# Kernel tuning notes

Measured on AMD Instinct MI355X. Metric: run time of the kernel, lower is better.

Reference implementation:

```python
import jax, jax.numpy as jnp
import numpy as np

N_NODES = 50000
N_EDGES = 1200000
IN_FEATS = 64
OUT_FEATS = 64
NEG_SLOPE = 0.01  # F.leaky_relu default


def setup_inputs() -> dict:
    key = jax.random.key(0)
    k1, k2, k3, k4, k5, k6 = jax.random.split(key, 6)
    feature = jax.random.normal(k1, (N_NODES, IN_FEATS), dtype=jnp.float32)
    attn_w = jax.random.normal(k2, (2 * IN_FEATS, 1), dtype=jnp.float32) * 0.1
    lin_w = jax.random.normal(k3, (OUT_FEATS, 2 * IN_FEATS), dtype=jnp.float32) * 0.1
    lin_b = jax.random.normal(k4, (OUT_FEATS,), dtype=jnp.float32) * 0.1
    src = jax.random.randint(k5, (N_EDGES,), 0, N_NODES, dtype=jnp.int32)
    dst = jax.random.randint(k6, (N_EDGES,), 0, N_NODES, dtype=jnp.int32)
    return {"feature": feature, "attn_w": attn_w, "lin_w": lin_w,
            "lin_b": lin_b, "src": src, "dst": dst}


def reference(feature, attn_w, lin_w, lin_b, src, dst):
    N = feature.shape[0]
    # edge attention: leaky_relu(attn_fc([h_src, h_dst]))
    # split attn weight to avoid materializing the [E, 2*in] concat
    a_src, a_dst = attn_w[:IN_FEATS, 0], attn_w[IN_FEATS:, 0]
    e = jax.nn.leaky_relu(feature[src] @ a_src + feature[dst] @ a_dst,
                          negative_slope=NEG_SLOPE)  # [E]
    # segment softmax over incoming edges of each destination node
    emax = jax.ops.segment_max(e, dst, num_segments=N)
    emax = jnp.where(jnp.isfinite(emax), emax, 0.0)  # guard empty segments
    ex = jnp.exp(e - emax[dst])                       # [E]
    denom = jax.ops.segment_sum(ex, dst, num_segments=N)          # [N]
    num = jax.ops.segment_sum(ex[:, None] * feature[src], dst,
                              num_segments=N)                      # [N, in]
    hm = jnp.where(denom[:, None] > 0, num / denom[:, None], 0.0)
    # node apply: relu(Linear([h, hm]))
    h = jnp.concatenate([feature, hm], axis=1) @ lin_w.T + lin_b
    return jax.nn.relu(h)
```

## Files before the change

kernel.cpp:

```cpp
#include <hip/hip_runtime.h>
#include <math.h>

#define N_NODES 50000
#define N_EDGES 1200000
#define F 64
#define CAP 49
#define BSTR2 56
#define OVF_MAX 1024
#define NBIN 782
#define BSTR 16
#define CAP_BIN 2304
#define TILE 8192
#define NTILE ((N_EDGES + TILE - 1) / TILE)
#define XSTR 72

typedef __attribute__((ext_vector_type(8))) short short8;
typedef __attribute__((ext_vector_type(4))) float v4f;


__device__ __forceinline__ unsigned short f32_to_bf16_rne(float f) {
    unsigned u = __float_as_uint(f);
    return (unsigned short)((u + 0x7FFFu + ((u >> 16) & 1u)) >> 16);
}

__global__ void k_prep(const float* __restrict__ feature,
                       const float* __restrict__ attn_w,
                       float* __restrict__ s, float* __restrict__ dd,
                       unsigned short* __restrict__ fb,
                       unsigned* __restrict__ fq32) {
    int gid = blockIdx.x * blockDim.x + threadIdx.x;
    int wave = gid >> 6;
    int lane = threadIdx.x & 63;
    if (wave >= N_NODES) return;
    float f = feature[wave * F + lane];
    fb[wave * F + lane] = f32_to_bf16_rne(f);
    if (lane < 16) {
        float4 x = ((const float4*)(feature + (size_t)wave * F))[lane];
        int pk0 = __builtin_amdgcn_cvt_pk_fp8_f32(x.x, x.y, 0, false);
        int pkw = __builtin_amdgcn_cvt_pk_fp8_f32(x.z, x.w, pk0, true);
        fq32[wave * 16 + lane] = (unsigned)pkw;
    }
    float sv = f * attn_w[lane];
    float dv = f * attn_w[F + lane];
    #pragma unroll
    for (int o = 32; o > 0; o >>= 1) {
        sv += __shfl_down(sv, o, 64);
        dv += __shfl_down(dv, o, 64);
    }
    if (lane == 0) {
        s[wave] = sv;
        dd[wave] = dv;
    }
}

__global__ __launch_bounds__(256) void k_bin(
        const int* __restrict__ src, const int* __restrict__ dst,
        int* __restrict__ bin_cnt, unsigned* __restrict__ binned) {
    __shared__ unsigned ord[TILE];
    __shared__ int cnt_l[NBIN], off_l[NBIN], cur_l[NBIN], base_g[NBIN];
    __shared__ int buf[256];
    int t = threadIdx.x;
    int e0 = blockIdx.x * TILE;
    int ecnt = N_EDGES - e0; if (ecnt > TILE) ecnt = TILE;
    for (int i = t; i < NBIN; i += 256) cnt_l[i] = 0;
    __syncthreads();
    int n4 = ecnt >> 2;
    const int4* s4p = (const int4*)src + (e0 >> 2);
    const int4* d4p = (const int4*)dst + (e0 >> 2);
    unsigned pk[32];
    int ng = 0;
    #pragma unroll
    for (int k = 0; k < 8; k++) {
        int c = t + k * 256;
        if (c < n4) {
            int4 d4 = d4p[c];
            int4 s4 = s4p[c];
            pk[4 * k + 0] = (((unsigned)d4.x) << 16) | (unsigned)s4.x;
            pk[4 * k + 1] = (((unsigned)d4.y) << 16) | (unsigned)s4.y;
            pk[4 * k + 2] = (((unsigned)d4.z) << 16) | (unsigned)s4.z;
            pk[4 * k + 3] = (((unsigned)d4.w) << 16) | (unsigned)s4.w;
            atomicAdd(&cnt_l[pk[4 * k + 0] >> 22], 1);
            atomicAdd(&cnt_l[pk[4 * k + 1] >> 22], 1);
            atomicAdd(&cnt_l[pk[4 * k + 2] >> 22], 1);
            atomicAdd(&cnt_l[pk[4 * k + 3] >> 22], 1);
            ng = k + 1;
        }
    }
    __syncthreads();
    int c0[4];
    int sum = 0;
    #pragma unroll
    for (int j = 0; j < 4; j++) {
        int idx = t * 4 + j;
        c0[j] = (idx < NBIN) ? cnt_l[idx] : 0;
        sum += c0[j];
    }
    buf[t] = sum;
    __syncthreads();
    #pragma unroll
    for (int d = 1; d < 256; d <<= 1) {
        int x = (t >= d) ? buf[t - d] : 0;
        __syncthreads();
        buf[t] += x;
        __syncthreads();
    }
    int excl = buf[t] - sum;
    #pragma unroll
    for (int j = 0; j < 4; j++) {
        int idx = t * 4 + j;
        if (idx < NBIN) {
            off_l[idx] = excl;
            cur_l[idx] = excl;
            base_g[idx] = atomicAdd(&bin_cnt[idx * BSTR], c0[j]);
        }
        excl += c0[j];
    }
    __syncthreads();
    for (int k = 0; k < ng; k++) {
        #pragma unroll
        for (int u = 0; u < 4; u++) {
            unsigned v = pk[4 * k + u];
            int r = atomicAdd(&cur_l[v >> 22], 1);
            ord[r] = v;
        }
    }
    __syncthreads();
    for (int i = t; i < ecnt; i += 256) {
        unsigned v = ord[i];
        int b = v >> 22;
        int pos = base_g[b] + (i - off_l[b]);
        if (pos < CAP_BIN) binned[(size_t)b * CAP_BIN + pos] = v;
    }
}

__global__ __launch_bounds__(256, 4) void k_fused(
        const unsigned* __restrict__ binned, const int* __restrict__ bin_cnt,
        int* __restrict__ cnt, unsigned short* __restrict__ bucket,
        int* __restrict__ ovf_cnt, unsigned* __restrict__ ovf,
        const float* __restrict__ s, const float* __restrict__ dd,
        const unsigned short* __restrict__ fb, const unsigned* __restrict__ fq32,
        const float* __restrict__ lin_w, const float* __restrict__ lin_b,
        float* __restrict__ out) {
    __shared__ int cnt_l[64];
    __shared__ __align__(16) unsigned short buck_l[64 * BSTR2];
    __shared__ unsigned short Wl[64 * 136];
    __shared__ __align__(16) unsigned short xl[4][16][XSTR];
    __shared__ __align__(16) float p_l[4][64];
    int t = threadIdx.x;
    int wid = t >> 6, lane = t & 63;
    int bin = blockIdx.x;
    int n0 = bin << 6;
    int nn = N_NODES - n0; if (nn > 64) nn = 64;
    for (int i = t; i < 64 * 128; i += 256)
        Wl[(i >> 7) * 136 + (i & 127)] = f32_to_bf16_rne(lin_w[i]);
    if (t < 64) cnt_l[t] = 0;
    {
        uint4 z4 = {0, 0, 0, 0};
        uint4* b4 = (uint4*)buck_l;
        for (int i = t; i < 448; i += 256) b4[i] = z4;
    }
    __syncthreads();
    int E = bin_cnt[bin * BSTR];
    if (E > CAP_BIN) E = CAP_BIN;
    const unsigned* be = binned + (size_t)bin * CAP_BIN;
    for (int i = t; i < E; i += 256) {
        unsigned v = be[i];
        int local = (v >> 16) & 63;
        int sid = (int)(v & 0xFFFFu);
        int r = atomicAdd(&cnt_l[local], 1);
        if (r < CAP) {
            buck_l[local * BSTR2 + r] = (unsigned short)sid;
        } else {
            int o = atomicAdd(ovf_cnt, 1);
            if (o < OVF_MAX)
                ovf[o] = ((unsigned)(n0 + local) << 16) | (unsigned)sid;
        }
    }
    __syncthreads();
    if (t < nn) {
        cnt[n0 + t] = cnt_l[t];
        if (cnt_l[t] > CAP) {
            for (int k2 = 0; k2 < CAP; k2++)
                bucket[(size_t)(n0 + t) * CAP + k2] = buck_l[t * BSTR2 + k2];
        }
    }
    __syncthreads();
    int grp = lane >> 4;
    int c16 = lane & 15;
    for (int j = 0; j < 16; j++) {
        int local = wid * 16 + j;
        if (local >= nn) break;
        int deg = cnt_l[local];
        if (deg == 0 || deg > CAP) {
            if (lane < 16) {
                ushort4 z = {0, 0, 0, 0};
                *(ushort4*)&xl[wid][j][lane * 4] = z;
            }
            continue;
        }
        float pr = 0.0f;
        if (lane < deg) {
            int si = (int)buck_l[local * BSTR2 + lane];
            float v = s[si] + dd[n0 + local];
            v = v > 0.0f ? v : 0.01f * v;
            pr = __expf(v);
        }
        float l = pr;
        #pragma unroll
        for (int o = 32; o > 0; o >>= 1)
            l += __shfl_xor(l, o, 64);
        p_l[wid][lane] = pr * __builtin_amdgcn_rcpf(l);
        float a0 = 0.0f, a1 = 0.0f, a2 = 0.0f, a3 = 0.0f;
        for (int e0 = 0; e0 < deg; e0 += 32) {
            ushort4 skA = *(const ushort4*)&buck_l[local * BSTR2 + e0 + grp * 8];
            ushort4 skB = *(const ushort4*)&buck_l[local * BSTR2 + e0 + grp * 8 + 4];
            float4 pA = *(const float4*)&p_l[wid][e0 + grp * 8];
            float4 pB = *(const float4*)&p_l[wid][e0 + grp * 8 + 4];
            unsigned wv[8];
            int sk[8] = {skA.x, skA.y, skA.z, skA.w, skB.x, skB.y, skB.z, skB.w};
            #pragma unroll
            for (int u = 0; u < 8; u++)
                wv[u] = fq32[sk[u] * 16 + c16];
            float pw[8] = {pA.x, pA.y, pA.z, pA.w, pB.x, pB.y, pB.z, pB.w};
            #pragma unroll
            for (int u = 0; u < 8; u++) {
                a0 = fmaf(pw[u], __builtin_amdgcn_cvt_f32_fp8(wv[u], 0), a0);
                a1 = fmaf(pw[u], __builtin_amdgcn_cvt_f32_fp8(wv[u], 1), a1);
                a2 = fmaf(pw[u], __builtin_amdgcn_cvt_f32_fp8(wv[u], 2), a2);
                a3 = fmaf(pw[u], __builtin_amdgcn_cvt_f32_fp8(wv[u], 3), a3);
            }
        }
        a0 += __shfl_xor(a0, 16, 64); a0 += __shfl_xor(a0, 32, 64);
        a1 += __shfl_xor(a1, 16, 64); a1 += __shfl_xor(a1, 32, 64);
        a2 += __shfl_xor(a2, 16, 64); a2 += __shfl_xor(a2, 32, 64);
        a3 += __shfl_xor(a3, 16, 64); a3 += __shfl_xor(a3, 32, 64);
        if (lane < 16) {
            ushort4 st;
            st.x = f32_to_bf16_rne(a0);
            st.y = f32_to_bf16_rne(a1);
            st.z = f32_to_bf16_rne(a2);
            st.w = f32_to_bf16_rne(a3);
            *(ushort4*)&xl[wid][j][c16 * 4] = st;
        }
    }
    int n0w = n0 + wid * 16;
    if (n0w >= N_NODES) return;
    int m = lane & 15, quad = lane >> 4;
    short8 afr[4];
    #pragma unroll
    for (int ks = 0; ks < 2; ks++) {
        int kb = ks * 32 + quad * 8;
        afr[ks] = *(const short8*)&fb[(size_t)(n0w + m) * F + kb];
    }
    #pragma unroll
    for (int ks = 2; ks < 4; ks++) {
        int kb = (ks - 2) * 32 + quad * 8;
        afr[ks] = *(const short8*)&xl[wid][m][kb];
    }
    #pragma unroll
    for (int nt = 0; nt < 4; nt++) {
        v4f acc = {0.0f, 0.0f, 0.0f, 0.0f};
        #pragma unroll
        for (int ks = 0; ks < 4; ks++) {
            int kb = ks * 32 + quad * 8;
            short8 b = *(const short8*)&Wl[(nt * 16 + m) * 136 + kb];
            acc = __builtin_amdgcn_mfma_f32_16x16x32_bf16(afr[ks], b, acc,
                                                          0, 0, 0);
        }
        int colo = nt * 16 + m;
        float bias = lin_b[colo];
        #pragma unroll
        for (int r = 0; r < 4; r++) {
            int row = quad * 4 + r;
            float v = acc[r] + bias;
            out[(size_t)(n0w + row) * F + colo] = fmaxf(v, 0.0f);
        }
    }
}

__global__ __launch_bounds__(256) void k_cleanup(
        const unsigned short* __restrict__ bucket,
        const int* __restrict__ cnt,
        const int* __restrict__ ovf_cnt, const unsigned int* __restrict__ ovf,
        const float* __restrict__ s, const float* __restrict__ dd,
        const float* __restrict__ feature,
        const float* __restrict__ lin_w, const float* __restrict__ lin_b,
        float* __restrict__ out) {
    int M = *ovf_cnt;
    if (M > OVF_MAX) M = OVF_MAX;
    if (M == 0) return;
    __shared__ float Wl[64 * 129];
    __shared__ int list[128];
    __shared__ int nlist;
    __shared__ unsigned short edg[4][256];
    __shared__ float xc[4][128];
    int t = threadIdx.x;
    for (int i = t; i < 64 * 128; i += 256)
        Wl[(i >> 7) * 129 + (i & 127)] = lin_w[i];
    if (t == 0) {
        nlist = 0;
        for (int i = 0; i < M; i++) {
            int d = (int)(ovf[i] >> 16);
            bool seen = false;
            for (int j = 0; j < nlist; j++) if (list[j] == d) seen = true;
            if (!seen && nlist < 128) list[nlist++] = d;
        }
    }
    __syncthreads();
    int wid = t >> 6, lane = t & 63;
    for (int idx = wid; idx < nlist; idx += 4) {
        int n = list[idx];
        int deg = cnt[n];
        if (lane < CAP) edg[wid][lane] = bucket[n * CAP + lane];
        int k2 = CAP;
        for (int base = 0; base < M; base += 64) {
            int i2 = base + lane;
            unsigned val = 0;
            bool mt = false;
            if (i2 < M) { val = ovf[i2]; mt = ((int)(val >> 16) == n); }
            unsigned long long mask = __ballot(mt);
            if (mt) {
                int pos = k2 + __popcll(mask & ((1ULL << lane) - 1ULL));
                if (pos < 256) edg[wid][pos] = (unsigned short)(val & 0xFFFFu);
            }
            k2 += __popcll(mask);
        }
        __threadfence_block();
        int nd = deg < 256 ? deg : 256;
        float m = -1e30f, l = 0.0f, acc = 0.0f;
        float dn = dd[n];
        for (int c0 = 0; c0 < nd; c0 += 64) {
            int j = c0 + lane;
            int sid = 0;
            float ev = -1e30f;
            if (j < nd) {
                sid = (int)edg[wid][j];
                float v = s[sid] + dn;
                ev = v > 0.0f ? v : 0.01f * v;
            }
            float cm = ev;
            #pragma unroll
            for (int o = 32; o > 0; o >>= 1)
                cm = fmaxf(cm, __shfl_xor(cm, o, 64));
            float np = (j < nd) ? __expf(ev - cm) : 0.0f;
            float cl = np;
            #pragma unroll
            for (int o = 32; o > 0; o >>= 1)
                cl += __shfl_xor(cl, o, 64);
            float cacc = 0.0f;
            int c = nd - c0; if (c > 64) c = 64;
            for (int k = 0; k < c; k += 16) {
                float fvv[16];
                #pragma unroll
                for (int u = 0; u < 16; u++) {
                    int sk = __builtin_amdgcn_readlane(sid, k + u);
                    fvv[u] = feature[sk * F + lane];
                }
                #pragma unroll
                for (int u = 0; u < 16; u++) {
                    float pk = __uint_as_float(
                        __builtin_amdgcn_readlane(__float_as_uint(np), k + u));
                    cacc = fmaf(pk, fvv[u], cacc);
                }
            }
            float mn = fmaxf(m, cm);
            float sc = __expf(m - mn);
            float sc2 = __expf(cm - mn);
            l = l * sc + cl * sc2;
            acc = acc * sc + cacc * sc2;
            m = mn;
        }
        float hm = acc / l;
        xc[wid][lane] = feature[n * F + lane];
        xc[wid][64 + lane] = hm;
        __threadfence_block();
        float oa = lin_b[lane];
        #pragma unroll
        for (int k = 0; k < 128; k++)
            oa += xc[wid][k] * Wl[lane * 129 + k];
        out[n * F + lane] = fmaxf(oa, 0.0f);
    }
}

extern "C" void kernel_launch(void* const* d_in, const int* in_sizes, int n_in,
                              void* d_out, int out_size, void* d_ws, size_t ws_size,
                              hipStream_t stream) {
    const float* feature = (const float*)d_in[0];
    const float* attn_w  = (const float*)d_in[1];
    const float* lin_w   = (const float*)d_in[2];
    const float* lin_b   = (const float*)d_in[3];
    const int*   src     = (const int*)d_in[4];
    const int*   dst     = (const int*)d_in[5];
    float* out = (float*)d_out;
    char* ws = (char*)d_ws;

    float*          s       = (float*)(ws);
    float*          dd      = (float*)(ws + 200000);
    int*            cnt     = (int*)  (ws + 400000);
    int*            bin_cnt = (int*)  (ws + 600000);
    int*            ovf_cnt = (int*)  (ws + 650048);
    unsigned*       ovf     = (unsigned*)(ws + 650112);
    unsigned short* bucket  = (unsigned short*)(ws + 654208);
    unsigned*       binned  = (unsigned*)(ws + 5554208);
    unsigned short* fb      = (unsigned short*)(ws + 12761120);
    unsigned*       fq32    = (unsigned*)(ws + 19161120);

    hipMemsetAsync(ws + 600000, 0, 50112, stream);
    k_prep<<<(N_NODES * 64) / 256, 256, 0, stream>>>(
        feature, attn_w, s, dd, fb, fq32);
    k_bin<<<NTILE, 256, 0, stream>>>(src, dst, bin_cnt, binned);
    k_fused<<<NBIN, 256, 0, stream>>>(
        binned, bin_cnt, cnt, bucket, ovf_cnt, ovf, s, dd, fb, fq32,
        lin_w, lin_b, out);
    k_cleanup<<<1, 256, 0, stream>>>(
        bucket, cnt, ovf_cnt, ovf, s, dd, feature, lin_w, lin_b, out);
}
```

Baseline: 140.2 us.

## Software-pipeline neighbor gathers, prequantize lin_w once, rotate bin atomics

```diff
diff --git a/kernel.cpp b/kernel.cpp
--- a/kernel.cpp
+++ b/kernel.cpp
@@ -13,6 +13,7 @@
 #define TILE 8192
 #define NTILE ((N_EDGES + TILE - 1) / TILE)
 #define XSTR 72
+#define PSTR 68
 
 typedef __attribute__((ext_vector_type(8))) short short8;
 typedef __attribute__((ext_vector_type(4))) float v4f;
@@ -25,10 +26,13 @@
 
 __global__ void k_prep(const float* __restrict__ feature,
                        const float* __restrict__ attn_w,
+                       const float* __restrict__ lin_w,
                        float* __restrict__ s, float* __restrict__ dd,
                        unsigned short* __restrict__ fb,
-                       unsigned* __restrict__ fq32) {
+                       unsigned* __restrict__ fq32,
+                       unsigned short* __restrict__ wq) {
     int gid = blockIdx.x * blockDim.x + threadIdx.x;
+    if (gid < 64 * 128) wq[gid] = f32_to_bf16_rne(lin_w[gid]);
     int wave = gid >> 6;
     int lane = threadIdx.x & 63;
     if (wave >= N_NODES) return;
@@ -111,9 +115,13 @@
         if (idx < NBIN) {
             off_l[idx] = excl;
             cur_l[idx] = excl;
-            base_g[idx] = atomicAdd(&bin_cnt[idx * BSTR], c0[j]);
         }
         excl += c0[j];
+    }
+    int rot = (int)((blockIdx.x * 389u) % NBIN);
+    for (int i = t; i < NBIN; i += 256) {
+        int idx = i + rot; if (idx >= NBIN) idx -= NBIN;
+        base_g[idx] = atomicAdd(&bin_cnt[idx * BSTR], cnt_l[idx]);
     }
     __syncthreads();
     for (int k = 0; k < ng; k++) {
@@ -139,20 +147,17 @@
         int* __restrict__ ovf_cnt, unsigned* __restrict__ ovf,
         const float* __restrict__ s, const float* __restrict__ dd,
         const unsigned short* __restrict__ fb, const unsigned* __restrict__ fq32,
-        const float* __restrict__ lin_w, const float* __restrict__ lin_b,
+        const unsigned short* __restrict__ wq, const float* __restrict__ lin_b,
         float* __restrict__ out) {
     __shared__ int cnt_l[64];
     __shared__ __align__(16) unsigned short buck_l[64 * BSTR2];
-    __shared__ unsigned short Wl[64 * 136];
     __shared__ __align__(16) unsigned short xl[4][16][XSTR];
-    __shared__ __align__(16) float p_l[4][64];
+    __shared__ __align__(16) float p_l[4][16][PSTR];
     int t = threadIdx.x;
     int wid = t >> 6, lane = t & 63;
     int bin = blockIdx.x;
     int n0 = bin << 6;
     int nn = N_NODES - n0; if (nn > 64) nn = 64;
-    for (int i = t; i < 64 * 128; i += 256)
-        Wl[(i >> 7) * 136 + (i & 127)] = f32_to_bf16_rne(lin_w[i]);
     if (t < 64) cnt_l[t] = 0;
     {
         uint4 z4 = {0, 0, 0, 0};
@@ -185,21 +190,13 @@
         }
     }
     __syncthreads();
-    int grp = lane >> 4;
-    int c16 = lane & 15;
+    #pragma unroll 2
     for (int j = 0; j < 16; j++) {
         int local = wid * 16 + j;
-        if (local >= nn) break;
-        int deg = cnt_l[local];
-        if (deg == 0 || deg > CAP) {
-            if (lane < 16) {
-                ushort4 z = {0, 0, 0, 0};
-                *(ushort4*)&xl[wid][j][lane * 4] = z;
-            }
-            continue;
-        }
+        int dg = cnt_l[local];
+        if (dg > CAP) dg = 0;
         float pr = 0.0f;
-        if (lane < deg) {
+        if (lane < dg) {
             int si = (int)buck_l[local * BSTR2 + lane];
             float v = s[si] + dd[n0 + local];
             v = v > 0.0f ? v : 0.01f * v;
@@ -209,25 +206,70 @@
         #pragma unroll
         for (int o = 32; o > 0; o >>= 1)
             l += __shfl_xor(l, o, 64);
-        p_l[wid][lane] = pr * __builtin_amdgcn_rcpf(l);
+        p_l[wid][j][lane] = pr * __builtin_amdgcn_rcpf(l + 1e-30f);
+    }
+    int grp = lane >> 4;
+    int c16 = lane & 15;
+    unsigned wvN[8];
+    float pwN[8];
+    {
+        int local = wid * 16;
+        ushort4 skA = *(const ushort4*)&buck_l[local * BSTR2 + grp * 8];
+        ushort4 skB = *(const ushort4*)&buck_l[local * BSTR2 + grp * 8 + 4];
+        float4 pA = *(const float4*)&p_l[wid][0][grp * 8];
+        float4 pB = *(const float4*)&p_l[wid][0][grp * 8 + 4];
+        int sk[8] = {skA.x, skA.y, skA.z, skA.w, skB.x, skB.y, skB.z, skB.w};
+        #pragma unroll
+        for (int u = 0; u < 8; u++) wvN[u] = fq32[sk[u] * 16 + c16];
+        pwN[0] = pA.x; pwN[1] = pA.y; pwN[2] = pA.z; pwN[3] = pA.w;
+        pwN[4] = pB.x; pwN[5] = pB.y; pwN[6] = pB.z; pwN[7] = pB.w;
+    }
+    #pragma unroll
+    for (int j = 0; j < 16; j++) {
+        unsigned wvC[8];
+        float pwC[8];
+        #pragma unroll
+        for (int u = 0; u < 8; u++) { wvC[u] = wvN[u]; pwC[u] = pwN[u]; }
+        if (j + 1 < 16) {
+            int local = wid * 16 + j + 1;
+            ushort4 skA = *(const ushort4*)&buck_l[local * BSTR2 + grp * 8];
+            ushort4 skB = *(const ushort4*)&buck_l[local * BSTR2 + grp * 8 + 4];
+            float4 pA = *(const float4*)&p_l[wid][j + 1][grp * 8];
+            float4 pB = *(const float4*)&p_l[wid][j + 1][grp * 8 + 4];
+            int sk[8] = {skA.x, skA.y, skA.z, skA.w,
+                         skB.x, skB.y, skB.z, skB.w};
+            #pragma unroll
+            for (int u = 0; u < 8; u++) wvN[u] = fq32[sk[u] * 16 + c16];
+            pwN[0] = pA.x; pwN[1] = pA.y; pwN[2] = pA.z; pwN[3] = pA.w;
+            pwN[4] = pB.x; pwN[5] = pB.y; pwN[6] = pB.z; pwN[7] = pB.w;
+        }
         float a0 = 0.0f, a1 = 0.0f, a2 = 0.0f, a3 = 0.0f;
-        for (int e0 = 0; e0 < deg; e0 += 32) {
-            ushort4 skA = *(const ushort4*)&buck_l[local * BSTR2 + e0 + grp * 8];
-            ushort4 skB = *(const ushort4*)&buck_l[local * BSTR2 + e0 + grp * 8 + 4];
-            float4 pA = *(const float4*)&p_l[wid][e0 + grp * 8];
-            float4 pB = *(const float4*)&p_l[wid][e0 + grp * 8 + 4];
-            unsigned wv[8];
-            int sk[8] = {skA.x, skA.y, skA.z, skA.w, skB.x, skB.y, skB.z, skB.w};
+        #pragma unroll
+        for (int u = 0; u < 8; u++) {
+            a0 = fmaf(pwC[u], __builtin_amdgcn_cvt_f32_fp8(wvC[u], 0), a0);
+            a1 = fmaf(pwC[u], __builtin_amdgcn_cvt_f32_fp8(wvC[u], 1), a1);
+            a2 = fmaf(pwC[u], __builtin_amdgcn_cvt_f32_fp8(wvC[u], 2), a2);
+            a3 = fmaf(pwC[u], __builtin_amdgcn_cvt_f32_fp8(wvC[u], 3), a3);
+        }
+        int dgj = cnt_l[wid * 16 + j];
+        if (dgj > 32 && dgj <= CAP) {
+            int local = wid * 16 + j;
+            ushort4 skA = *(const ushort4*)&buck_l[local * BSTR2 + 32 + grp * 8];
+            ushort4 skB = *(const ushort4*)&buck_l[local * BSTR2 + 36 + grp * 8];
+            float4 pA = *(const float4*)&p_l[wid][j][32 + grp * 8];
+            float4 pB = *(const float4*)&p_l[wid][j][36 + grp * 8];
+            int sk[8] = {skA.x, skA.y, skA.z, skA.w,
+                         skB.x, skB.y, skB.z, skB.w};
+            unsigned wv2[8];
             #pragma unroll
-            for (int u = 0; u < 8; u++)
-                wv[u] = fq32[sk[u] * 16 + c16];
-            float pw[8] = {pA.x, pA.y, pA.z, pA.w, pB.x, pB.y, pB.z, pB.w};
+            for (int u = 0; u < 8; u++) wv2[u] = fq32[sk[u] * 16 + c16];
+            float pw2[8] = {pA.x, pA.y, pA.z, pA.w, pB.x, pB.y, pB.z, pB.w};
             #pragma unroll
             for (int u = 0; u < 8; u++) {
-                a0 = fmaf(pw[u], __builtin_amdgcn_cvt_f32_fp8(wv[u], 0), a0);
-                a1 = fmaf(pw[u], __builtin_amdgcn_cvt_f32_fp8(wv[u], 1), a1);
-                a2 = fmaf(pw[u], __builtin_amdgcn_cvt_f32_fp8(wv[u], 2), a2);
-                a3 = fmaf(pw[u], __builtin_amdgcn_cvt_f32_fp8(wv[u], 3), a3);
+                a0 = fmaf(pw2[u], __builtin_amdgcn_cvt_f32_fp8(wv2[u], 0), a0);
+                a1 = fmaf(pw2[u], __builtin_amdgcn_cvt_f32_fp8(wv2[u], 1), a1);
+                a2 = fmaf(pw2[u], __builtin_amdgcn_cvt_f32_fp8(wv2[u], 2), a2);
+                a3 = fmaf(pw2[u], __builtin_amdgcn_cvt_f32_fp8(wv2[u], 3), a3);
             }
         }
         a0 += __shfl_xor(a0, 16, 64); a0 += __shfl_xor(a0, 32, 64);
@@ -263,7 +305,7 @@
         #pragma unroll
         for (int ks = 0; ks < 4; ks++) {
             int kb = ks * 32 + quad * 8;
-            short8 b = *(const short8*)&Wl[(nt * 16 + m) * 136 + kb];
+            short8 b = *(const short8*)&wq[(nt * 16 + m) * 128 + kb];
             acc = __builtin_amdgcn_mfma_f32_16x16x32_bf16(afr[ks], b, acc,
                                                           0, 0, 0);
         }
@@ -404,14 +446,15 @@
     unsigned*       binned  = (unsigned*)(ws + 5554208);
     unsigned short* fb      = (unsigned short*)(ws + 12761120);
     unsigned*       fq32    = (unsigned*)(ws + 19161120);
+    unsigned short* wq      = (unsigned short*)(ws + 22361120);
 
     hipMemsetAsync(ws + 600000, 0, 50112, stream);
     k_prep<<<(N_NODES * 64) / 256, 256, 0, stream>>>(
-        feature, attn_w, s, dd, fb, fq32);
+        feature, attn_w, lin_w, s, dd, fb, fq32, wq);
     k_bin<<<NTILE, 256, 0, stream>>>(src, dst, bin_cnt, binned);
     k_fused<<<NBIN, 256, 0, stream>>>(
         binned, bin_cnt, cnt, bucket, ovf_cnt, ovf, s, dd, fb, fq32,
-        lin_w, lin_b, out);
+        wq, lin_b, out);
     k_cleanup<<<1, 256, 0, stream>>>(
         bucket, cnt, ovf_cnt, ovf, s, dd, feature, lin_w, lin_b, out);
 }
```

New measurement: 139.5 us. Within noise of the previous version (-0.5%).
